# Kernel tuning notes

Measured on AMD Instinct MI355X. Metric: run time of the kernel, lower is better.

The kernel has to match this reference:

```python
import jax, jax.numpy as jnp
import numpy as np

B, S, HID, NH = 4, 2048, 1024, 16
HD = HID // NH  # head_dim = 64


def setup_inputs() -> dict:
    key = jax.random.key(0)
    ks = jax.random.split(key, 5)
    scale = 0.02
    return {
        "hidden_states": jax.random.normal(ks[0], (B, S, HID), dtype=jnp.float32),
        "attention_mask": jnp.zeros((B, 1, 1, S), dtype=jnp.float32),
        "Wq": jax.random.normal(ks[1], (HID, HID), dtype=jnp.float32) * scale,
        "bq": jnp.zeros((HID,), dtype=jnp.float32),
        "Wk": jax.random.normal(ks[2], (HID, HID), dtype=jnp.float32) * scale,
        "bk": jnp.zeros((HID,), dtype=jnp.float32),
        "Wv": jax.random.normal(ks[3], (HID, HID), dtype=jnp.float32) * scale,
        "bv": jnp.zeros((HID,), dtype=jnp.float32),
    }


def _split_heads(x):
    # [B, S, HID] -> [B, NH, S, HD]
    b, s, _ = x.shape
    return x.reshape(b, s, NH, HD).transpose(0, 2, 1, 3)


def reference(hidden_states, attention_mask, Wq, bq, Wk, bk, Wv, bv):
    # Linear projections (torch Linear: x @ W.T + b)
    q = _split_heads(hidden_states @ Wq.T + bq)
    k = _split_heads(hidden_states @ Wk.T + bk)
    v = _split_heads(hidden_states @ Wv.T + bv)

    # scores: [B, NH, S, S]
    scores = jnp.einsum("bhqd,bhkd->bhqk", q, k) / jnp.sqrt(jnp.float32(HD))
    scores = scores + attention_mask  # additive mask, broadcast over heads/query
    weights = jax.nn.softmax(scores, axis=-1)
    # dropout prob = 0 (inference), head_mask = None

    context = jnp.einsum("bhqk,bhkd->bhqd", weights, v)
    # [B, NH, S, HD] -> [B, S, HID]
    context = context.transpose(0, 2, 1, 3).reshape(hidden_states.shape[0], hidden_states.shape[1], HID)
    return context
```

## Files before the change

### kernel.cpp

```cpp
#include <hip/hip_runtime.h>
#include <stdint.h>


typedef float f32x4 __attribute__((ext_vector_type(4)));
typedef float f32x16 __attribute__((ext_vector_type(16)));
typedef __bf16 bf16x8 __attribute__((ext_vector_type(8)));
typedef unsigned short ushort_t;
typedef uint32_t u32;

#define MFMA16(a, b, c) __builtin_amdgcn_mfma_f32_16x16x32_bf16(a, b, c, 0, 0, 0)
#define MFMA32(a, b, c) __builtin_amdgcn_mfma_f32_32x32x16_bf16(a, b, c, 0, 0, 0)

__device__ __forceinline__ ushort_t f2b(float f) {
    union { float f; uint32_t u; } x{f};
    uint32_t r = (x.u + 0x7fffu + ((x.u >> 16) & 1u)) >> 16;
    return (ushort_t)r;
}

__device__ __forceinline__ float fexp2(float x) {
#if __has_builtin(__builtin_amdgcn_exp2f)
    return __builtin_amdgcn_exp2f(x);
#else
    return exp2f(x);
#endif
}

__device__ __forceinline__ u32 pkpair(float e, float o) {
    union { float f; u32 u; } xe{e}, xo{o};
    return __builtin_amdgcn_perm(xo.u, xe.u, 0x07060302u);
}

__device__ __forceinline__ bf16x8 mk8(u32 a, u32 b, u32 c, u32 d) {
    union { u32 u[4]; bf16x8 v; } x;
    x.u[0] = a; x.u[1] = b; x.u[2] = c; x.u[3] = d;
    return x.v;
}

__device__ __forceinline__ void gld_lds16(const void* g, void* l) {
    __builtin_amdgcn_global_load_lds(
        (const __attribute__((address_space(1))) unsigned int*)g,
        (__attribute__((address_space(3))) unsigned int*)l, 16, 0, 0);
}

__global__ __launch_bounds__(256) void convert_k(
    const float* __restrict__ hs, const float* __restrict__ wq,
    const float* __restrict__ wk, const float* __restrict__ wv,
    ushort_t* __restrict__ hs_b, ushort_t* __restrict__ w_b) {
    size_t c = (size_t)blockIdx.x * 256 + threadIdx.x;
    size_t i = c * 8;
    const size_t NHS = (size_t)8192 * 1024;
    const float* src;
    ushort_t* dst;
    if (i < NHS) { src = hs + i; dst = hs_b + i; }
    else {
        size_t j = i - NHS;
        int w = (int)(j >> 20);
        size_t o = j & ((1u << 20) - 1);
        src = (w == 0 ? wq : (w == 1 ? wk : wv)) + o;
        dst = w_b + ((size_t)w << 20) + o;
    }
    float4 a = *(const float4*)src;
    float4 b = *(const float4*)(src + 4);
    uint32_t p0 = (uint32_t)f2b(a.x) | ((uint32_t)f2b(a.y) << 16);
    uint32_t p1 = (uint32_t)f2b(a.z) | ((uint32_t)f2b(a.w) << 16);
    uint32_t p2 = (uint32_t)f2b(b.x) | ((uint32_t)f2b(b.y) << 16);
    uint32_t p3 = (uint32_t)f2b(b.z) | ((uint32_t)f2b(b.w) << 16);
    uint4 v{p0, p1, p2, p3};
    *(uint4*)dst = v;
}

__global__ __launch_bounds__(256, 2) void qkv_gemm(
    const ushort_t* __restrict__ Ab, const ushort_t* __restrict__ Wb,
    const float* __restrict__ bq, const float* __restrict__ bk,
    const float* __restrict__ bv, ushort_t* __restrict__ q_ws,
    ushort_t* __restrict__ k_ws, ushort_t* __restrict__ vt_ws) {
    __shared__ __align__(16) char smem_raw[128 * 136 * 2];
    ushort_t* At = (ushort_t*)smem_raw;
    ushort_t* Bt = At + 128 * 64;
    ushort_t* Ct = (ushort_t*)smem_raw;
    int which = blockIdx.z;
    const ushort_t* W = Wb + ((size_t)which << 20);
    int m0 = blockIdx.y * 128, n0 = blockIdx.x * 128;
    int t = threadIdx.x, lane = t & 63, wave = t >> 6;
    int quad = lane >> 4, l16 = lane & 15;
    int wr = (wave >> 1) * 64, wc = (wave & 1) * 64;
    f32x4 acc[4][4] = {};
    for (int k0 = 0; k0 < 1024; k0 += 64) {
        for (int r = 0; r < 4; r++) {
            int idx = r * 256 + t;
            int row = idx >> 3, co = (idx & 7) * 8;
            gld_lds16(Ab + (size_t)(m0 + row) * 1024 + k0 + co, At + idx * 8);
            gld_lds16(W + (size_t)(n0 + row) * 1024 + k0 + co, Bt + idx * 8);
        }
        asm volatile("s_waitcnt vmcnt(0)" ::: "memory");
        __syncthreads();
        for (int kk = 0; kk < 2; kk++) {
            bf16x8 af[4], bf[4];
            for (int i = 0; i < 4; i++)
                af[i] = *(const bf16x8*)(At + (wr + i * 16 + l16) * 64 + kk * 32 + quad * 8);
            for (int j = 0; j < 4; j++)
                bf[j] = *(const bf16x8*)(Bt + (wc + j * 16 + l16) * 64 + kk * 32 + quad * 8);
            for (int i = 0; i < 4; i++)
                for (int j = 0; j < 4; j++)
                    acc[i][j] = MFMA16(af[i], bf[j], acc[i][j]);
        }
        __syncthreads();
    }
    const float* bias = which == 0 ? bq : (which == 1 ? bk : bv);
    float sc = which == 0 ? (0.125f * 1.44269504f) : 1.0f;
    if (which == 2) {
        for (int j = 0; j < 4; j++) {
            float bias_v = bias[n0 + wc + j * 16 + l16];
            for (int i = 0; i < 4; i++) {
                ushort4 pk;
                pk.x = f2b(acc[i][j].x + bias_v);
                pk.y = f2b(acc[i][j].y + bias_v);
                pk.z = f2b(acc[i][j].z + bias_v);
                pk.w = f2b(acc[i][j].w + bias_v);
                *(ushort4*)(Ct + (wc + j * 16 + l16) * 136 + wr + i * 16 + quad * 4) = pk;
            }
        }
    } else {
        for (int j = 0; j < 4; j++) {
            float bias_v = bias[n0 + wc + j * 16 + l16];
            int col = wc + j * 16 + l16;
            for (int i = 0; i < 4; i++) {
                int rb = wr + i * 16 + quad * 4;
                Ct[(rb + 0) * 136 + col] = f2b((acc[i][j].x + bias_v) * sc);
                Ct[(rb + 1) * 136 + col] = f2b((acc[i][j].y + bias_v) * sc);
                Ct[(rb + 2) * 136 + col] = f2b((acc[i][j].z + bias_v) * sc);
                Ct[(rb + 3) * 136 + col] = f2b((acc[i][j].w + bias_v) * sc);
            }
        }
    }
    __syncthreads();
    for (int r = 0; r < 8; r++) {
        int idx = r * 256 + t;
        int row = idx >> 4, c8 = (idx & 15) * 8;
        uint4 val = *(const uint4*)(Ct + row * 136 + c8);
        if (which == 2) {
            int col = n0 + row, h = col >> 6, d = col & 63;
            int tok = m0 + c8, b = tok >> 11, s = tok & 2047;
            *(uint4*)(vt_ws + ((size_t)(b * 16 + h) * 64 + d) * 2048 + s) = val;
        } else {
            int tok = m0 + row, b = tok >> 11, s = tok & 2047;
            int col = n0 + c8, h = col >> 6, d = col & 63;
            ushort_t* base = which == 0 ? q_ws : k_ws;
            *(uint4*)(base + ((size_t)(b * 16 + h) * 2048 + s) * 64 + d) = val;
        }
    }
}

__global__ __launch_bounds__(256, 2) void attn_k(
    const ushort_t* __restrict__ q_ws, const ushort_t* __restrict__ k_ws,
    const ushort_t* __restrict__ vt_ws, const float* __restrict__ mask,
    float* __restrict__ out) {
    __shared__ __align__(16) char smraw[33280];
    ushort_t* Kl = (ushort_t*)smraw;
    ushort_t* Vtl = Kl + 64 * 64;
    float* Ow = (float*)smraw;

    int bh = blockIdx.y, b = bh >> 4, h = bh & 15;
    int q0 = blockIdx.x * 256;
    int t = threadIdx.x, lane = t & 63, w = t >> 6;
    int l31 = lane & 31, hi = lane >> 5;
    bool h0 = (hi == 0);
    const ushort_t* Q = q_ws + (size_t)bh * 2048 * 64;
    const ushort_t* K = k_ws + (size_t)bh * 2048 * 64;
    const ushort_t* Vt = vt_ws + (size_t)bh * 64 * 2048;
    const float* mrow = mask + b * 2048;

    bf16x8 qf[2][4];
#pragma unroll
    for (int qg = 0; qg < 2; qg++)
#pragma unroll
        for (int cs = 0; cs < 4; cs++)
            qf[qg][cs] = *(const bf16x8*)(
                Q + (size_t)(q0 + w * 64 + qg * 32 + l31) * 64 + cs * 16 + hi * 8);
    int co[4];
#pragma unroll
    for (int cs = 0; cs < 4; cs++) co[cs] = ((cs * 2 + hi) ^ (l31 & 7)) * 8;

    f32x16 o00 = {}, o01 = {}, o10 = {}, o11 = {};
    float rs0 = 0.f, rs1 = 0.f;

    for (int t0 = 0; t0 < 2048; t0 += 64) {
#pragma unroll
        for (int it = 0; it < 2; it++) {
            int idx = it * 256 + t;
            int row = idx >> 3, ch = idx & 7;
            int sch = (ch ^ (row & 7)) * 8;
            gld_lds16(K + (size_t)(t0 + row) * 64 + sch, Kl + idx * 8);
            gld_lds16(Vt + (size_t)row * 2048 + t0 + sch, Vtl + idx * 8);
        }
        asm volatile("s_waitcnt vmcnt(0)" ::: "memory");
        __syncthreads();
        f32x16 s00 = {}, s01 = {}, s10 = {}, s11 = {};
#pragma unroll
        for (int cs = 0; cs < 4; cs++) {
            bf16x8 k0 = *(const bf16x8*)(Kl + l31 * 64 + co[cs]);
            bf16x8 k1 = *(const bf16x8*)(Kl + (32 + l31) * 64 + co[cs]);
            s00 = MFMA32(k0, qf[0][cs], s00);
            s01 = MFMA32(k1, qf[0][cs], s01);
            s10 = MFMA32(k0, qf[1][cs], s10);
            s11 = MFMA32(k1, qf[1][cs], s11);
        }
        bf16x8 pfr[2][4];
#pragma unroll
        for (int qg = 0; qg < 2; qg++) {
            const f32x16& sa = qg ? s10 : s00;
            const f32x16& sb = qg ? s11 : s01;
            u32 pa[8], pb[8];
            float rst = 0.f;
#pragma unroll
            for (int i = 0; i < 4; i++) {
                float4 bm = *(const float4*)(mrow + t0 + 8 * i + 4 * hi);
                float e0 = fexp2(fmaf(bm.x, 1.44269504f, sa[4 * i + 0]));
                float e1 = fexp2(fmaf(bm.y, 1.44269504f, sa[4 * i + 1]));
                float e2 = fexp2(fmaf(bm.z, 1.44269504f, sa[4 * i + 2]));
                float e3 = fexp2(fmaf(bm.w, 1.44269504f, sa[4 * i + 3]));
                rst += (e0 + e1) + (e2 + e3);
                pa[2 * i] = pkpair(e0, e1);
                pa[2 * i + 1] = pkpair(e2, e3);
            }
#pragma unroll
            for (int i = 0; i < 4; i++) {
                float4 bm = *(const float4*)(mrow + t0 + 32 + 8 * i + 4 * hi);
                float e0 = fexp2(fmaf(bm.x, 1.44269504f, sb[4 * i + 0]));
                float e1 = fexp2(fmaf(bm.y, 1.44269504f, sb[4 * i + 1]));
                float e2 = fexp2(fmaf(bm.z, 1.44269504f, sb[4 * i + 2]));
                float e3 = fexp2(fmaf(bm.w, 1.44269504f, sb[4 * i + 3]));
                rst += (e0 + e1) + (e2 + e3);
                pb[2 * i] = pkpair(e0, e1);
                pb[2 * i + 1] = pkpair(e2, e3);
            }
            if (qg == 0) rs0 += rst; else rs1 += rst;
#pragma unroll
            for (int g = 0; g < 4; g++) {
                const u32* aa = (g < 2) ? pa : pb;
                int base = (g & 1) * 4;
                u32 y0 = h0 ? aa[base + 2] : aa[base + 0];
                u32 y1 = h0 ? aa[base + 3] : aa[base + 1];
                u32 sy0 = (u32)__shfl_xor((int)y0, 32, 64);
                u32 sy1 = (u32)__shfl_xor((int)y1, 32, 64);
                pfr[qg][g] = mk8(h0 ? aa[base + 0] : sy0, h0 ? aa[base + 1] : sy1,
                                 h0 ? sy0 : aa[base + 2], h0 ? sy1 : aa[base + 3]);
            }
        }
#pragma unroll
        for (int cs = 0; cs < 4; cs++) {
            bf16x8 v0 = *(const bf16x8*)(Vtl + l31 * 64 + co[cs]);
            bf16x8 v1 = *(const bf16x8*)(Vtl + (32 + l31) * 64 + co[cs]);
            o00 = MFMA32(v0, pfr[0][cs], o00);
            o01 = MFMA32(v1, pfr[0][cs], o01);
            o10 = MFMA32(v0, pfr[1][cs], o10);
            o11 = MFMA32(v1, pfr[1][cs], o11);
        }
        __syncthreads();
    }
    rs0 += __shfl_xor(rs0, 32, 64);
    rs1 += __shfl_xor(rs1, 32, 64);
    float inv0 = 1.f / rs0, inv1 = 1.f / rs1;
#pragma unroll
    for (int qg = 0; qg < 2; qg++) {
        float inv = qg ? inv1 : inv0;
        const f32x16& a0 = qg ? o10 : o00;
        const f32x16& a1 = qg ? o11 : o01;
#pragma unroll
        for (int g = 0; g < 4; g++) {
            f32x4 c0, c1;
#pragma unroll
            for (int r = 0; r < 4; r++) {
                c0[r] = a0[4 * g + r] * inv;
                c1[r] = a1[4 * g + r] * inv;
            }
            *(f32x4*)(Ow + (w * 32 + l31) * 65 + 8 * g + 4 * hi) = c0;
            *(f32x4*)(Ow + (w * 32 + l31) * 65 + 32 + 8 * g + 4 * hi) = c1;
        }
        __syncthreads();
#pragma unroll
        for (int cc = 0; cc < 8; cc++) {
            int c = cc * 256 + t;
            int row = c >> 4, seg = (c & 15) * 4;
            f32x4 vv = *(const f32x4*)(Ow + row * 65 + seg);
            int ql = (row >> 5) * 64 + qg * 32 + (row & 31);
            *(f32x4*)(out + ((size_t)(b * 2048 + q0 + ql)) * 1024 + h * 64 + seg) = vv;
        }
        __syncthreads();
    }
}

extern "C" void kernel_launch(void* const* d_in, const int* in_sizes, int n_in,
                              void* d_out, int out_size, void* d_ws, size_t ws_size,
                              hipStream_t stream) {
    const float* hs = (const float*)d_in[0];
    const float* mask = (const float*)d_in[1];
    const float* wq = (const float*)d_in[2];
    const float* bq = (const float*)d_in[3];
    const float* wk = (const float*)d_in[4];
    const float* bk = (const float*)d_in[5];
    const float* wv = (const float*)d_in[6];
    const float* bv = (const float*)d_in[7];
    float* out = (float*)d_out;
    char* ws = (char*)d_ws;
    ushort_t* hs_b = (ushort_t*)ws;
    ushort_t* w_b = (ushort_t*)(ws + 16777216);
    ushort_t* q_ws = (ushort_t*)(ws + 23068672);
    ushort_t* k_ws = (ushort_t*)(ws + 39845888);
    ushort_t* vt_ws = (ushort_t*)(ws + 56623104);

    convert_k<<<5632, 256, 0, stream>>>(hs, wq, wk, wv, hs_b, w_b);
    qkv_gemm<<<dim3(8, 64, 3), 256, 0, stream>>>(hs_b, w_b, bq, bk, bv, q_ws, k_ws, vt_ws);
    attn_k<<<dim3(8, 64), 256, 0, stream>>>(q_ws, k_ws, vt_ws, mask, out);
}
```

Before: 256.9 us.

## Double-buffer K/V tiles in LDS with 128-key tiles and prefetch

The attention loop now stages 128-key tiles of K and V^T into two LDS buffers and prefetches the next tile while computing on the current one. This replaces one global-load wait and two barriers per 64 keys with one wait and one barrier per 128 keys, and overlaps load latency with MFMA and exp work. The V^T swizzle is widened to 16 chunks to fit 128-wide rows. LDS use rises to 64 KB per block, which may lower occupancy below the launch-bounds target of two blocks per CU.

```diff
diff --git a/kernel.cpp b/kernel.cpp
--- a/kernel.cpp
+++ b/kernel.cpp
@@ -155,9 +155,7 @@
     const ushort_t* __restrict__ q_ws, const ushort_t* __restrict__ k_ws,
     const ushort_t* __restrict__ vt_ws, const float* __restrict__ mask,
     float* __restrict__ out) {
-    __shared__ __align__(16) char smraw[33280];
-    ushort_t* Kl = (ushort_t*)smraw;
-    ushort_t* Vtl = Kl + 64 * 64;
+    __shared__ __align__(16) char smraw[65536];
     float* Ow = (float*)smraw;
 
     int bh = blockIdx.y, b = bh >> 4, h = bh & 15;
@@ -184,83 +182,101 @@
     f32x16 o00 = {}, o01 = {}, o10 = {}, o11 = {};
     float rs0 = 0.f, rs1 = 0.f;
 
-    for (int t0 = 0; t0 < 2048; t0 += 64) {
-#pragma unroll
-        for (int it = 0; it < 2; it++) {
+    auto stage = [&](int bufi, int t0) {
+        ushort_t* Klb = (ushort_t*)(smraw + bufi * 32768);
+        ushort_t* Vtlb = Klb + 8192;
+#pragma unroll
+        for (int it = 0; it < 4; it++) {
             int idx = it * 256 + t;
-            int row = idx >> 3, ch = idx & 7;
-            int sch = (ch ^ (row & 7)) * 8;
-            gld_lds16(K + (size_t)(t0 + row) * 64 + sch, Kl + idx * 8);
-            gld_lds16(Vt + (size_t)row * 2048 + t0 + sch, Vtl + idx * 8);
-        }
+            int krow = idx >> 3, kch = idx & 7;
+            gld_lds16(K + (size_t)(t0 + krow) * 64 + ((kch ^ (krow & 7)) * 8),
+                      Klb + idx * 8);
+            int vrow = idx >> 4, vch = idx & 15;
+            gld_lds16(Vt + (size_t)vrow * 2048 + t0 + ((vch ^ (vrow & 15)) * 8),
+                      Vtlb + idx * 8);
+        }
+    };
+
+    stage(0, 0);
+    int buf = 0;
+    for (int t0 = 0; t0 < 2048; t0 += 128) {
         asm volatile("s_waitcnt vmcnt(0)" ::: "memory");
         __syncthreads();
-        f32x16 s00 = {}, s01 = {}, s10 = {}, s11 = {};
-#pragma unroll
-        for (int cs = 0; cs < 4; cs++) {
-            bf16x8 k0 = *(const bf16x8*)(Kl + l31 * 64 + co[cs]);
-            bf16x8 k1 = *(const bf16x8*)(Kl + (32 + l31) * 64 + co[cs]);
-            s00 = MFMA32(k0, qf[0][cs], s00);
-            s01 = MFMA32(k1, qf[0][cs], s01);
-            s10 = MFMA32(k0, qf[1][cs], s10);
-            s11 = MFMA32(k1, qf[1][cs], s11);
-        }
-        bf16x8 pfr[2][4];
-#pragma unroll
-        for (int qg = 0; qg < 2; qg++) {
-            const f32x16& sa = qg ? s10 : s00;
-            const f32x16& sb = qg ? s11 : s01;
-            u32 pa[8], pb[8];
-            float rst = 0.f;
-#pragma unroll
-            for (int i = 0; i < 4; i++) {
-                float4 bm = *(const float4*)(mrow + t0 + 8 * i + 4 * hi);
-                float e0 = fexp2(fmaf(bm.x, 1.44269504f, sa[4 * i + 0]));
-                float e1 = fexp2(fmaf(bm.y, 1.44269504f, sa[4 * i + 1]));
-                float e2 = fexp2(fmaf(bm.z, 1.44269504f, sa[4 * i + 2]));
-                float e3 = fexp2(fmaf(bm.w, 1.44269504f, sa[4 * i + 3]));
-                rst += (e0 + e1) + (e2 + e3);
-                pa[2 * i] = pkpair(e0, e1);
-                pa[2 * i + 1] = pkpair(e2, e3);
-            }
-#pragma unroll
-            for (int i = 0; i < 4; i++) {
-                float4 bm = *(const float4*)(mrow + t0 + 32 + 8 * i + 4 * hi);
-                float e0 = fexp2(fmaf(bm.x, 1.44269504f, sb[4 * i + 0]));
-                float e1 = fexp2(fmaf(bm.y, 1.44269504f, sb[4 * i + 1]));
-                float e2 = fexp2(fmaf(bm.z, 1.44269504f, sb[4 * i + 2]));
-                float e3 = fexp2(fmaf(bm.w, 1.44269504f, sb[4 * i + 3]));
-                rst += (e0 + e1) + (e2 + e3);
-                pb[2 * i] = pkpair(e0, e1);
-                pb[2 * i + 1] = pkpair(e2, e3);
-            }
-            if (qg == 0) rs0 += rst; else rs1 += rst;
-#pragma unroll
-            for (int g = 0; g < 4; g++) {
-                const u32* aa = (g < 2) ? pa : pb;
-                int base = (g & 1) * 4;
-                u32 y0 = h0 ? aa[base + 2] : aa[base + 0];
-                u32 y1 = h0 ? aa[base + 3] : aa[base + 1];
-                u32 sy0 = (u32)__shfl_xor((int)y0, 32, 64);
-                u32 sy1 = (u32)__shfl_xor((int)y1, 32, 64);
-                pfr[qg][g] = mk8(h0 ? aa[base + 0] : sy0, h0 ? aa[base + 1] : sy1,
-                                 h0 ? sy0 : aa[base + 2], h0 ? sy1 : aa[base + 3]);
-            }
-        }
-#pragma unroll
-        for (int cs = 0; cs < 4; cs++) {
-            bf16x8 v0 = *(const bf16x8*)(Vtl + l31 * 64 + co[cs]);
-            bf16x8 v1 = *(const bf16x8*)(Vtl + (32 + l31) * 64 + co[cs]);
-            o00 = MFMA32(v0, pfr[0][cs], o00);
-            o01 = MFMA32(v1, pfr[0][cs], o01);
-            o10 = MFMA32(v0, pfr[1][cs], o10);
-            o11 = MFMA32(v1, pfr[1][cs], o11);
-        }
-        __syncthreads();
+        if (t0 + 128 < 2048) stage(buf ^ 1, t0 + 128);
+        ushort_t* Klb = (ushort_t*)(smraw + buf * 32768);
+        ushort_t* Vtlb = Klb + 8192;
+#pragma unroll
+        for (int kh = 0; kh < 2; kh++) {
+            int kb = kh * 64;
+            f32x16 s00 = {}, s01 = {}, s10 = {}, s11 = {};
+#pragma unroll
+            for (int cs = 0; cs < 4; cs++) {
+                bf16x8 k0 = *(const bf16x8*)(Klb + (kb + l31) * 64 + co[cs]);
+                bf16x8 k1 = *(const bf16x8*)(Klb + (kb + 32 + l31) * 64 + co[cs]);
+                s00 = MFMA32(k0, qf[0][cs], s00);
+                s01 = MFMA32(k1, qf[0][cs], s01);
+                s10 = MFMA32(k0, qf[1][cs], s10);
+                s11 = MFMA32(k1, qf[1][cs], s11);
+            }
+            bf16x8 pfr[2][4];
+#pragma unroll
+            for (int qg = 0; qg < 2; qg++) {
+                const f32x16& sa = qg ? s10 : s00;
+                const f32x16& sb = qg ? s11 : s01;
+                u32 pa[8], pb[8];
+                float rst = 0.f;
+#pragma unroll
+                for (int i = 0; i < 4; i++) {
+                    float4 bm = *(const float4*)(mrow + t0 + kb + 8 * i + 4 * hi);
+                    float e0 = fexp2(fmaf(bm.x, 1.44269504f, sa[4 * i + 0]));
+                    float e1 = fexp2(fmaf(bm.y, 1.44269504f, sa[4 * i + 1]));
+                    float e2 = fexp2(fmaf(bm.z, 1.44269504f, sa[4 * i + 2]));
+                    float e3 = fexp2(fmaf(bm.w, 1.44269504f, sa[4 * i + 3]));
+                    rst += (e0 + e1) + (e2 + e3);
+                    pa[2 * i] = pkpair(e0, e1);
+                    pa[2 * i + 1] = pkpair(e2, e3);
+                }
+#pragma unroll
+                for (int i = 0; i < 4; i++) {
+                    float4 bm = *(const float4*)(mrow + t0 + kb + 32 + 8 * i + 4 * hi);
+                    float e0 = fexp2(fmaf(bm.x, 1.44269504f, sb[4 * i + 0]));
+                    float e1 = fexp2(fmaf(bm.y, 1.44269504f, sb[4 * i + 1]));
+                    float e2 = fexp2(fmaf(bm.z, 1.44269504f, sb[4 * i + 2]));
+                    float e3 = fexp2(fmaf(bm.w, 1.44269504f, sb[4 * i + 3]));
+                    rst += (e0 + e1) + (e2 + e3);
+                    pb[2 * i] = pkpair(e0, e1);
+                    pb[2 * i + 1] = pkpair(e2, e3);
+                }
+                if (qg == 0) rs0 += rst; else rs1 += rst;
+#pragma unroll
+                for (int g = 0; g < 4; g++) {
+                    const u32* aa = (g < 2) ? pa : pb;
+                    int base = (g & 1) * 4;
+                    u32 y0 = h0 ? aa[base + 2] : aa[base + 0];
+                    u32 y1 = h0 ? aa[base + 3] : aa[base + 1];
+                    u32 sy0 = (u32)__shfl_xor((int)y0, 32, 64);
+                    u32 sy1 = (u32)__shfl_xor((int)y1, 32, 64);
+                    pfr[qg][g] = mk8(h0 ? aa[base + 0] : sy0, h0 ? aa[base + 1] : sy1,
+                                     h0 ? sy0 : aa[base + 2], h0 ? sy1 : aa[base + 3]);
+                }
+            }
+#pragma unroll
+            for (int cs = 0; cs < 4; cs++) {
+                int vc0 = ((kh * 8 + cs * 2 + hi) ^ (l31 & 15)) * 8;
+                bf16x8 v0 = *(const bf16x8*)(Vtlb + l31 * 128 + vc0);
+                bf16x8 v1 = *(const bf16x8*)(Vtlb + (32 + l31) * 128 + vc0);
+                o00 = MFMA32(v0, pfr[0][cs], o00);
+                o01 = MFMA32(v1, pfr[0][cs], o01);
+                o10 = MFMA32(v0, pfr[1][cs], o10);
+                o11 = MFMA32(v1, pfr[1][cs], o11);
+            }
+        }
+        buf ^= 1;
     }
     rs0 += __shfl_xor(rs0, 32, 64);
     rs1 += __shfl_xor(rs1, 32, 64);
     float inv0 = 1.f / rs0, inv1 = 1.f / rs1;
+    __syncthreads();
 #pragma unroll
     for (int qg = 0; qg < 2; qg++) {
         float inv = qg ? inv1 : inv0;
```

New measurement: 350.2 us. 36.3% more time.
